# Kernel tuning notes

Hardware: AMD Instinct MI355X
Metric: run time of the kernel (lower is better)

## Reference

```python
import jax, jax.numpy as jnp
import numpy as np

N_NODES = 100000
N_EDGES = 1600000
HID = 64


def setup_inputs() -> dict:
    key = jax.random.key(0)
    ks = jax.random.split(key, 16)
    s = 0.05
    inp = {
        "x": jax.random.normal(ks[0], (N_NODES, HID), dtype=jnp.float32),
        "edge_index": jax.random.randint(ks[1], (2, N_EDGES), 0, N_NODES, dtype=jnp.int32),
        # GatedGraphConv (num_layers=1): weight shape [out, out], used as x @ W
        "W_conv": jax.random.normal(ks[2], (HID, HID), dtype=jnp.float32) * s,
        # torch.nn.GRUCell params (gate order: r, z, n)
        "gru_w_ih": jax.random.normal(ks[3], (3 * HID, HID), dtype=jnp.float32) * s,
        "gru_w_hh": jax.random.normal(ks[4], (3 * HID, HID), dtype=jnp.float32) * s,
        "gru_b_ih": jax.random.normal(ks[5], (3 * HID,), dtype=jnp.float32) * s,
        "gru_b_hh": jax.random.normal(ks[6], (3 * HID,), dtype=jnp.float32) * s,
        # torch.nn.LSTM single layer params (gate order: i, f, g, o)
        "lstm_w_ih": jax.random.normal(ks[7], (4 * HID, HID), dtype=jnp.float32) * s,
        "lstm_w_hh": jax.random.normal(ks[8], (4 * HID, HID), dtype=jnp.float32) * s,
        "lstm_b_ih": jax.random.normal(ks[9], (4 * HID,), dtype=jnp.float32) * s,
        "lstm_b_hh": jax.random.normal(ks[10], (4 * HID,), dtype=jnp.float32) * s,
        # output Linear(hidden, hidden)
        "lin_w": jax.random.normal(ks[11], (HID, HID), dtype=jnp.float32) * s,
        "lin_b": jax.random.normal(ks[12], (HID,), dtype=jnp.float32) * s,
    }
    return inp


def _sigmoid(v):
    return jax.nn.sigmoid(v)


def reference(x, edge_index, W_conv, gru_w_ih, gru_w_hh, gru_b_ih, gru_b_hh,
              lstm_w_ih, lstm_w_hh, lstm_b_ih, lstm_b_hh, lin_w, lin_b):
    N = x.shape[0]
    H = W_conv.shape[0]
    # --- GatedGraphConv(out=H, num_layers=1, aggr='mean') ---
    # pad features to out_channels if needed (no-op here since input_dim == H)
    if x.shape[1] < H:
        x = jnp.pad(x, ((0, 0), (0, H - x.shape[1])))
    m = x @ W_conv                                    # [N, H]
    src, dst = edge_index[0], edge_index[1]
    # mean aggregation of source messages at destination nodes
    agg = jax.ops.segment_sum(m[src], dst, num_segments=N)          # [N, H]
    cnt = jax.ops.segment_sum(jnp.ones_like(src, dtype=m.dtype), dst, num_segments=N)
    agg = agg / jnp.maximum(cnt, 1.0)[:, None]
    # GRUCell(agg, x): gates r, z, n
    gi = agg @ gru_w_ih.T + gru_b_ih                  # [N, 3H]
    gh = x @ gru_w_hh.T + gru_b_hh                    # [N, 3H]
    ir, iz, inn = jnp.split(gi, 3, axis=1)
    hr, hz, hn = jnp.split(gh, 3, axis=1)
    r = _sigmoid(ir + hr)
    z = _sigmoid(iz + hz)
    n = jnp.tanh(inn + r * hn)
    h_conv = (1.0 - z) * n + z * x                    # [N, H]
    # --- LSTM (1 layer, seq_len=1, zero initial (H, C)) ---
    gates = h_conv @ lstm_w_ih.T + lstm_b_ih + lstm_b_hh   # h0 = 0 -> W_hh @ h0 = 0
    gi_, gf_, gg_, go_ = jnp.split(gates, 4, axis=1)
    c = _sigmoid(gi_) * jnp.tanh(gg_)                 # f * c0 = 0
    h_tilde = _sigmoid(go_) * jnp.tanh(c)             # [N, H]
    # --- ReLU + Linear ---
    out = jax.nn.relu(h_tilde) @ lin_w.T + lin_b      # [N, H]
    return out
```

## Files before the change

### kernel.cpp

```cpp
#include <hip/hip_runtime.h>
#include <math.h>

#define N_NODES 100000
#define N_EDGES 1600000
#define PAD_DEG 64

typedef __bf16 bf16_t;
typedef __attribute__((ext_vector_type(8))) __bf16 bf16x8;
typedef __attribute__((ext_vector_type(4))) __bf16 bf16x4;
typedef __attribute__((ext_vector_type(4))) float f32x4;

#define GT_WHH  0
#define GT_WIH  12
#define GT_LSTM 24
#define GT_LIN  36
#define N_GT    40
#define PACK_ELEMS (N_GT * 1024)
#define CAST_BLOCKS ((N_NODES * 16 + 16 + 255) / 256)
#define PACK_BLOCKS ((PACK_ELEMS + 255) / 256)

#define NODES_PER_RANGE 12500
#define PLACE_GROUP 304
#define PLACE_BLOCKS (8 * PLACE_GROUP)

__device__ __forceinline__ float sigm(float v) { return 1.f / (1.f + __expf(-v)); }
__device__ __forceinline__ float tanh_(float v) { return 2.f * sigm(2.f * v) - 1.f; }

__device__ __forceinline__ void split8(const float* __restrict__ p, bf16x8& hi, bf16x8& lo) {
    f32x4 a = *(const f32x4*)p;
    f32x4 b = *(const f32x4*)(p + 4);
#pragma unroll
    for (int i = 0; i < 4; ++i) {
        float v = a[i];
        __bf16 h = (__bf16)v;
        hi[i] = h;
        lo[i] = (__bf16)(v - (float)h);
        v = b[i];
        h = (__bf16)v;
        hi[4 + i] = h;
        lo[4 + i] = (__bf16)(v - (float)h);
    }
}

__device__ __forceinline__ bf16x8 zero8() {
    bf16x8 r;
#pragma unroll
    for (int i = 0; i < 8; ++i) r[i] = (__bf16)0.f;
    return r;
}

__device__ __forceinline__ f32x4 mm6(f32x4 acc, bf16x8 ah0, bf16x8 ah1, bf16x8 al0, bf16x8 al1,
                                     const bf16_t* __restrict__ ph, const bf16_t* __restrict__ pl,
                                     int gt, int l) {
    const bf16x8 bh0 = *(const bf16x8*)(ph + (gt * 2 + 0) * 512 + l * 8);
    const bf16x8 bh1 = *(const bf16x8*)(ph + (gt * 2 + 1) * 512 + l * 8);
    const bf16x8 bl0 = *(const bf16x8*)(pl + (gt * 2 + 0) * 512 + l * 8);
    const bf16x8 bl1 = *(const bf16x8*)(pl + (gt * 2 + 1) * 512 + l * 8);
    acc = __builtin_amdgcn_mfma_f32_16x16x32_bf16(ah0, bh0, acc, 0, 0, 0);
    acc = __builtin_amdgcn_mfma_f32_16x16x32_bf16(ah1, bh1, acc, 0, 0, 0);
    acc = __builtin_amdgcn_mfma_f32_16x16x32_bf16(al0, bh0, acc, 0, 0, 0);
    acc = __builtin_amdgcn_mfma_f32_16x16x32_bf16(al1, bh1, acc, 0, 0, 0);
    acc = __builtin_amdgcn_mfma_f32_16x16x32_bf16(ah0, bl0, acc, 0, 0, 0);
    acc = __builtin_amdgcn_mfma_f32_16x16x32_bf16(ah1, bl1, acc, 0, 0, 0);
    return acc;
}

__global__ __launch_bounds__(256) void k_pre(const float* __restrict__ x, bf16_t* __restrict__ xb,
                                             const float* __restrict__ Wc,
                                             const float* __restrict__ wih,
                                             const float* __restrict__ whh,
                                             const float* __restrict__ lw,
                                             const float* __restrict__ lin,
                                             bf16_t* __restrict__ ph, bf16_t* __restrict__ pl,
                                             const int* __restrict__ ei,
                                             int* __restrict__ cnt, int* __restrict__ ss) {
    int b = blockIdx.x;
    if (b < PLACE_BLOCKS) {
        int r = b & 7, gi = b >> 3;
        int lo = r * NODES_PER_RANGE;
        int hi = lo + NODES_PER_RANGE;
        for (int e = gi * 256 + threadIdx.x; e < N_EDGES; e += PLACE_GROUP * 256) {
            int d = ei[N_EDGES + e];
            if (d >= lo && d < hi) {
                int s = ei[e];
                int p = atomicAdd(&cnt[d], 1);
                if (p < PAD_DEG) ss[d * PAD_DEG + p] = s;
            }
        }
        return;
    }
    b -= PLACE_BLOCKS;
    if (b < CAST_BLOCKS) {
        int t = b * 256 + threadIdx.x;
        if (t < N_NODES * 16) {
            f32x4 v = *(const f32x4*)(x + (size_t)t * 4);
            bf16x4 o;
#pragma unroll
            for (int i = 0; i < 4; ++i) o[i] = (__bf16)v[i];
            *(bf16x4*)(xb + (size_t)t * 4) = o;
        } else if (t < N_NODES * 16 + 16) {
            bf16x4 o;
#pragma unroll
            for (int i = 0; i < 4; ++i) o[i] = (__bf16)0.f;
            *(bf16x4*)(xb + (size_t)t * 4) = o;
        }
        return;
    }
    b -= CAST_BLOCKS;
    int t = b * 256 + threadIdx.x;
    if (t >= PACK_ELEMS) return;
    int i = t & 7, lane = (t >> 3) & 63, kk = (t >> 9) & 1, gt = t >> 10;
    int f = lane & 15;
    int k = kk * 32 + (lane >> 4) * 8 + i;
    float v;
    if (gt < 12) {
        v = whh[(gt * 16 + f) * 64 + k];
    } else if (gt < 24) {
        int j = (gt - 12) * 16 + f;
        float acc = 0.f;
        for (int c = 0; c < 64; ++c) acc += Wc[k * 64 + c] * wih[j * 64 + c];
        v = acc;
    } else if (gt < 36) {
        int jg = (gt - 24) * 16 + f;
        int row = (jg < 64) ? jg : jg + 64;
        v = lw[row * 64 + k];
    } else {
        v = lin[((gt - 36) * 16 + f) * 64 + k];
    }
    __bf16 h = (__bf16)v;
    ph[t] = h;
    pl[t] = (__bf16)(v - (float)h);
}

__global__ __launch_bounds__(256) void k_fused(
    const float* __restrict__ x, const bf16_t* __restrict__ xb,
    const int* __restrict__ ss, const int* __restrict__ cnt,
    const bf16_t* __restrict__ ph, const bf16_t* __restrict__ pl,
    const float* __restrict__ b_ih, const float* __restrict__ b_hh,
    const float* __restrict__ lb_ih, const float* __restrict__ lb_hh,
    const float* __restrict__ lin_b, float* __restrict__ out) {
    __shared__ float sc[4 * 16 * 68];
    int tid = threadIdx.x, w = tid >> 6, l = tid & 63;
    int base = blockIdx.x * 64 + w * 16;
    float* sw = &sc[w * 16 * 68];
    int f16 = l & 15, k0 = (l >> 4) * 8, hq = l >> 4;

    int g = l >> 4;
    int f4 = (l & 15) * 4;
    int dcl = 0;
    if (l < 16 && base + l < N_NODES) dcl = cnt[base + l];
    if (dcl > PAD_DEG) dcl = PAD_DEG;

    int idxq = 0;
    if (base < N_NODES) idxq = ss[(size_t)base * PAD_DEG + l];

#pragma unroll 1
    for (int t = 0; t < 16; ++t) {
        int dc = __shfl(dcl, t, 64);
        int idxv = (l < dc) ? idxq : N_NODES;
        if (t < 15 && base + t + 1 < N_NODES) idxq = ss[(size_t)(base + t + 1) * PAD_DEG + l];
        float a0 = 0.f, a1 = 0.f, a2 = 0.f, a3 = 0.f;

#define GLD(name, sb) \
        int s##name = __shfl(idxv, (sb) + g, 64); \
        bf16x4 v##name = *(const bf16x4*)(xb + (size_t)s##name * 64 + f4);
#define GACC(name) \
        a0 += (float)v##name[0]; a1 += (float)v##name[1]; \
        a2 += (float)v##name[2]; a3 += (float)v##name[3];

        if (dc <= 16) {
            GLD(A, 0) GLD(B, 4) GLD(C, 8) GLD(D, 12)
            GACC(A) GACC(B) GACC(C) GACC(D)
        } else {
            GLD(A, 0) GLD(B, 4) GLD(C, 8) GLD(D, 12)
            GLD(E, 16) GLD(F, 20) GLD(G, 24) GLD(H, 28)
            GACC(A) GACC(B) GACC(C) GACC(D)
            GACC(E) GACC(F) GACC(G) GACC(H)
            for (int e = 32 + g; e < dc; e += 4) {
                int s_ = __shfl(idxv, e, 64);
                bf16x4 v_ = *(const bf16x4*)(xb + (size_t)s_ * 64 + f4);
                a0 += (float)v_[0]; a1 += (float)v_[1];
                a2 += (float)v_[2]; a3 += (float)v_[3];
            }
        }
#undef GLD
#undef GACC
        a0 += __shfl_xor(a0, 16, 64); a0 += __shfl_xor(a0, 32, 64);
        a1 += __shfl_xor(a1, 16, 64); a1 += __shfl_xor(a1, 32, 64);
        a2 += __shfl_xor(a2, 16, 64); a2 += __shfl_xor(a2, 32, 64);
        a3 += __shfl_xor(a3, 16, 64); a3 += __shfl_xor(a3, 32, 64);
        float inv = 1.f / fmaxf((float)dc, 1.f);
        if (l < 16) {
            f32x4 o = {a0 * inv, a1 * inv, a2 * inv, a3 * inv};
            *(f32x4*)&sw[t * 68 + f4] = o;
        }
    }

    bf16x8 ah0, al0, ah1, al1;
    split8(&sw[f16 * 68 + k0], ah0, al0);
    split8(&sw[f16 * 68 + 32 + k0], ah1, al1);

    bf16x8 xh0 = zero8(), xl0 = zero8(), xh1 = zero8(), xl1 = zero8();
    {
        int xrow = base + f16;
        if (xrow < N_NODES) {
            split8(&x[xrow * 64 + k0], xh0, xl0);
            split8(&x[xrow * 64 + 32 + k0], xh1, xl1);
        }
    }

#pragma unroll 1
    for (int jj = 0; jj < 4; ++jj) {
        float bhr = b_hh[jj * 16 + f16], bhz = b_hh[64 + jj * 16 + f16], bhn = b_hh[128 + jj * 16 + f16];
        f32x4 ghr = {bhr, bhr, bhr, bhr}, ghz = {bhz, bhz, bhz, bhz}, ghn = {bhn, bhn, bhn, bhn};
        ghr = mm6(ghr, xh0, xh1, xl0, xl1, ph, pl, GT_WHH + jj, l);
        ghz = mm6(ghz, xh0, xh1, xl0, xl1, ph, pl, GT_WHH + 4 + jj, l);
        ghn = mm6(ghn, xh0, xh1, xl0, xl1, ph, pl, GT_WHH + 8 + jj, l);
        __builtin_amdgcn_sched_barrier(0);
        float bir = b_ih[jj * 16 + f16], biz = b_ih[64 + jj * 16 + f16], bin_ = b_ih[128 + jj * 16 + f16];
        f32x4 gir = {bir, bir, bir, bir}, giz = {biz, biz, biz, biz}, gin = {bin_, bin_, bin_, bin_};
        gir = mm6(gir, ah0, ah1, al0, al1, ph, pl, GT_WIH + jj, l);
        giz = mm6(giz, ah0, ah1, al0, al1, ph, pl, GT_WIH + 4 + jj, l);
        gin = mm6(gin, ah0, ah1, al0, al1, ph, pl, GT_WIH + 8 + jj, l);
        __builtin_amdgcn_sched_barrier(0);
#pragma unroll
        for (int rr = 0; rr < 4; ++rr) {
            int row = base + hq * 4 + rr;
            float xc = (row < N_NODES) ? x[row * 64 + jj * 16 + f16] : 0.f;
            float gr = sigm(gir[rr] + ghr[rr]);
            float gz = sigm(giz[rr] + ghz[rr]);
            float gn = tanh_(gin[rr] + gr * ghn[rr]);
            sw[(hq * 4 + rr) * 68 + jj * 16 + f16] = (1.f - gz) * gn + gz * xc;
        }
    }

    bf16x8 hh0, hl0, hh1, hl1;
    split8(&sw[f16 * 68 + k0], hh0, hl0);
    split8(&sw[f16 * 68 + 32 + k0], hh1, hl1);

#pragma unroll 1
    for (int jj = 0; jj < 4; ++jj) {
        float bi = lb_ih[jj * 16 + f16] + lb_hh[jj * 16 + f16];
        float bg = lb_ih[128 + jj * 16 + f16] + lb_hh[128 + jj * 16 + f16];
        float bo = lb_ih[192 + jj * 16 + f16] + lb_hh[192 + jj * 16 + f16];
        f32x4 ai = {bi, bi, bi, bi}, ag = {bg, bg, bg, bg}, ao = {bo, bo, bo, bo};
        ai = mm6(ai, hh0, hh1, hl0, hl1, ph, pl, GT_LSTM + jj, l);
        ag = mm6(ag, hh0, hh1, hl0, hl1, ph, pl, GT_LSTM + 4 + jj, l);
        ao = mm6(ao, hh0, hh1, hl0, hl1, ph, pl, GT_LSTM + 8 + jj, l);
        __builtin_amdgcn_sched_barrier(0);
#pragma unroll
        for (int rr = 0; rr < 4; ++rr) {
            float c = sigm(ai[rr]) * tanh_(ag[rr]);
            float ht = sigm(ao[rr]) * tanh_(c);
            sw[(hq * 4 + rr) * 68 + jj * 16 + f16] = fmaxf(ht, 0.f);
        }
    }

    bf16x8 rh0, rl0, rh1, rl1;
    split8(&sw[f16 * 68 + k0], rh0, rl0);
    split8(&sw[f16 * 68 + 32 + k0], rh1, rl1);

#pragma unroll 1
    for (int jj = 0; jj < 4; ++jj) {
        float bb = lin_b[jj * 16 + f16];
        f32x4 acc = {bb, bb, bb, bb};
        acc = mm6(acc, rh0, rh1, rl0, rl1, ph, pl, GT_LIN + jj, l);
#pragma unroll
        for (int rr = 0; rr < 4; ++rr) {
            int row = base + hq * 4 + rr;
            if (row < N_NODES) __builtin_nontemporal_store(acc[rr], &out[row * 64 + jj * 16 + f16]);
        }
    }
}

extern "C" void kernel_launch(void* const* d_in, const int* in_sizes, int n_in,
                              void* d_out, int out_size, void* d_ws, size_t ws_size,
                              hipStream_t stream) {
    const float* x    = (const float*)d_in[0];
    const int*   ei   = (const int*)d_in[1];
    const float* Wc   = (const float*)d_in[2];
    const float* gwih = (const float*)d_in[3];
    const float* gwhh = (const float*)d_in[4];
    const float* gbih = (const float*)d_in[5];
    const float* gbhh = (const float*)d_in[6];
    const float* lwih = (const float*)d_in[7];
    const float* lbih = (const float*)d_in[9];
    const float* lbhh = (const float*)d_in[10];
    const float* linw = (const float*)d_in[11];
    const float* linb = (const float*)d_in[12];
    float* out = (float*)d_out;

    int*    ss  = (int*)d_ws;
    int*    cnt = ss + (size_t)N_NODES * PAD_DEG;
    bf16_t* ph  = (bf16_t*)(cnt + N_NODES);
    bf16_t* pl  = ph + PACK_ELEMS;
    bf16_t* xb  = pl + PACK_ELEMS;

    hipMemsetAsync(cnt, 0, (size_t)N_NODES * sizeof(int), stream);

    dim3 b(256);
    k_pre<<<dim3(PLACE_BLOCKS + CAST_BLOCKS + PACK_BLOCKS), b, 0, stream>>>(
        x, xb, Wc, gwih, gwhh, lwih, linw, ph, pl, ei, cnt, ss);
    k_fused<<<dim3((N_NODES + 63) / 64), b, 0, stream>>>(
        x, xb, ss, cnt, ph, pl, gbih, gbhh, lbih, lbhh, linb, out);
}
```

Before: 174.7 us.

## Partition edges into destination-range buckets before scattering into padded adjacency

Before the change, each of eight node ranges re-read the whole edge list and kept only the edges whose destination fell in its range. Now a partition kernel reads the edges once, groups them in shared memory into eight destination buckets, and writes each bucket to global memory in wave-sized chunks, packing source and local destination into one int. A new scatter kernel then reads each bucket and fills the padded adjacency using atomics on nodes within a single range. This cuts redundant edge reads at the cost of an extra kernel launch and an intermediate buffer, whose fixed bucket capacity could overflow if destinations were skewed.

```diff
diff --git a/kernel.cpp b/kernel.cpp
--- a/kernel.cpp
+++ b/kernel.cpp
@@ -20,8 +20,10 @@
 #define PACK_BLOCKS ((PACK_ELEMS + 255) / 256)
 
 #define NODES_PER_RANGE 12500
-#define PLACE_GROUP 304
-#define PLACE_BLOCKS (8 * PLACE_GROUP)
+#define BUCKET_CAP 204800
+#define EPB 2048
+#define PART_BLOCKS ((N_EDGES + EPB - 1) / EPB)
+#define SCAT_GROUP 256
 
 __device__ __forceinline__ float sigm(float v) { return 1.f / (1.f + __expf(-v)); }
 __device__ __forceinline__ float tanh_(float v) { return 2.f * sigm(2.f * v) - 1.f; }
@@ -65,31 +67,70 @@
     return acc;
 }
 
-__global__ __launch_bounds__(256) void k_pre(const float* __restrict__ x, bf16_t* __restrict__ xb,
-                                             const float* __restrict__ Wc,
-                                             const float* __restrict__ wih,
-                                             const float* __restrict__ whh,
-                                             const float* __restrict__ lw,
-                                             const float* __restrict__ lin,
-                                             bf16_t* __restrict__ ph, bf16_t* __restrict__ pl,
-                                             const int* __restrict__ ei,
-                                             int* __restrict__ cnt, int* __restrict__ ss) {
+__global__ __launch_bounds__(256) void k_part(const int* __restrict__ ei,
+                                              int* __restrict__ gcur, int* __restrict__ gbuf,
+                                              const float* __restrict__ x, bf16_t* __restrict__ xb,
+                                              const float* __restrict__ Wc,
+                                              const float* __restrict__ wih,
+                                              const float* __restrict__ whh,
+                                              const float* __restrict__ lw,
+                                              const float* __restrict__ lin,
+                                              bf16_t* __restrict__ ph, bf16_t* __restrict__ pl) {
     int b = blockIdx.x;
-    if (b < PLACE_BLOCKS) {
-        int r = b & 7, gi = b >> 3;
-        int lo = r * NODES_PER_RANGE;
-        int hi = lo + NODES_PER_RANGE;
-        for (int e = gi * 256 + threadIdx.x; e < N_EDGES; e += PLACE_GROUP * 256) {
-            int d = ei[N_EDGES + e];
-            if (d >= lo && d < hi) {
+    if (b < PART_BLOCKS) {
+        __shared__ int lbuf[8][320];
+        __shared__ int lcnt[8];
+        int tid = threadIdx.x, lane = tid & 63, wv = tid >> 6;
+        if (tid < 8) lcnt[tid] = 0;
+        __syncthreads();
+        int e0 = b * EPB;
+        int e1 = e0 + EPB;
+        if (e1 > N_EDGES) e1 = N_EDGES;
+        for (int ebase = e0; ebase < e1; ebase += 256) {
+            int e = ebase + tid;
+            if (e < e1) {
+                int d = ei[N_EDGES + e];
                 int s = ei[e];
-                int p = atomicAdd(&cnt[d], 1);
-                if (p < PAD_DEG) ss[d * PAD_DEG + p] = s;
+                unsigned bkt = ((unsigned)((unsigned)d * 42950u)) >> 29;
+                int idx = atomicAdd(&lcnt[bkt], 1);
+                lbuf[bkt][idx] = (s << 14) | (d - (int)bkt * NODES_PER_RANGE);
             }
+            __syncthreads();
+#pragma unroll
+            for (int bb = 0; bb < 2; ++bb) {
+                int bkt = wv + bb * 4;
+                int c = lcnt[bkt];
+                int nf = c & ~63;
+                if (nf > 0) {
+                    int gb = 0;
+                    if (lane == 0) gb = atomicAdd(&gcur[bkt], nf);
+                    gb = __shfl(gb, 0, 64);
+                    for (int i = lane; i < nf; i += 64)
+                        gbuf[(size_t)bkt * BUCKET_CAP + gb + i] = lbuf[bkt][i];
+                    int rem = c - nf;
+                    int tmp = 0;
+                    if (lane < rem) tmp = lbuf[bkt][nf + lane];
+                    if (lane < rem) lbuf[bkt][lane] = tmp;
+                    if (lane == 0) lcnt[bkt] = rem;
+                }
+            }
+            __syncthreads();
+        }
+#pragma unroll
+        for (int bb = 0; bb < 2; ++bb) {
+            int bkt = wv + bb * 4;
+            int c = lcnt[bkt];
+            if (c > 0) {
+                int gb = 0;
+                if (lane == 0) gb = atomicAdd(&gcur[bkt], c);
+                gb = __shfl(gb, 0, 64);
+                if (lane < c)
+                    gbuf[(size_t)bkt * BUCKET_CAP + gb + lane] = lbuf[bkt][lane];
+            }
         }
         return;
     }
-    b -= PLACE_BLOCKS;
+    b -= PART_BLOCKS;
     if (b < CAST_BLOCKS) {
         int t = b * 256 + threadIdx.x;
         if (t < N_NODES * 16) {
@@ -132,6 +173,23 @@
     pl[t] = (__bf16)(v - (float)h);
 }
 
+__global__ __launch_bounds__(256) void k_scat(const int* __restrict__ gbuf,
+                                              const int* __restrict__ gcur,
+                                              int* __restrict__ cnt, int* __restrict__ ss) {
+    int r = blockIdx.x & 7, gi = blockIdx.x >> 3;
+    int n = gcur[r];
+    if (n > BUCKET_CAP) n = BUCKET_CAP;
+    int base = r * NODES_PER_RANGE;
+    const int* gb = gbuf + (size_t)r * BUCKET_CAP;
+    for (int i = gi * 256 + threadIdx.x; i < n; i += SCAT_GROUP * 256) {
+        int v = gb[i];
+        int d = base + (v & 0x3FFF);
+        int s = v >> 14;
+        int p = atomicAdd(&cnt[d], 1);
+        if (p < PAD_DEG) ss[d * PAD_DEG + p] = s;
+    }
+}
+
 __global__ __launch_bounds__(256) void k_fused(
     const float* __restrict__ x, const bf16_t* __restrict__ xb,
     const int* __restrict__ ss, const int* __restrict__ cnt,
@@ -290,17 +348,20 @@
     const float* linb = (const float*)d_in[12];
     float* out = (float*)d_out;
 
-    int*    ss  = (int*)d_ws;
-    int*    cnt = ss + (size_t)N_NODES * PAD_DEG;
-    bf16_t* ph  = (bf16_t*)(cnt + N_NODES);
-    bf16_t* pl  = ph + PACK_ELEMS;
-    bf16_t* xb  = pl + PACK_ELEMS;
-
-    hipMemsetAsync(cnt, 0, (size_t)N_NODES * sizeof(int), stream);
+    int*    ss   = (int*)d_ws;
+    int*    cnt  = ss + (size_t)N_NODES * PAD_DEG;
+    int*    gcur = cnt + N_NODES;
+    bf16_t* ph   = (bf16_t*)(gcur + 8);
+    bf16_t* pl   = ph + PACK_ELEMS;
+    bf16_t* xb   = pl + PACK_ELEMS;
+    int*    gbuf = (int*)(xb + (size_t)(N_NODES + 1) * 64);
+
+    hipMemsetAsync(cnt, 0, (size_t)(N_NODES + 8) * sizeof(int), stream);
 
     dim3 b(256);
-    k_pre<<<dim3(PLACE_BLOCKS + CAST_BLOCKS + PACK_BLOCKS), b, 0, stream>>>(
-        x, xb, Wc, gwih, gwhh, lwih, linw, ph, pl, ei, cnt, ss);
+    k_part<<<dim3(PART_BLOCKS + CAST_BLOCKS + PACK_BLOCKS), b, 0, stream>>>(
+        ei, gcur, gbuf, x, xb, Wc, gwih, gwhh, lwih, linw, ph, pl);
+    k_scat<<<dim3(8 * SCAT_GROUP), b, 0, stream>>>(gbuf, gcur, cnt, ss);
     k_fused<<<dim3((N_NODES + 63) / 64), b, 0, stream>>>(
         x, xb, ss, cnt, ph, pl, gbih, gbhh, lbih, lbhh, linb, out);
 }
```

New measurement: 496.9 us. +184.4%, slower.
